# Kernel tuning notes

Hardware: AMD Instinct MI355X
Metric: run time of the kernel (lower is better)

## Reference

```python
import jax, jax.numpy as jnp
import numpy as np

R = 32          # voxel_resolution
GN_GROUPS = 8   # GroupNorm groups used throughout the module


def group_norm(x, scale, bias, groups, eps=1e-5):
    B, C = x.shape[0], x.shape[1]
    spatial = x.shape[2:]
    xg = x.reshape(B, groups, C // groups, -1)
    mu = xg.mean(axis=(2, 3), keepdims=True)
    var = xg.var(axis=(2, 3), keepdims=True)
    xn = ((xg - mu) / jnp.sqrt(var + eps)).reshape((B, C) + spatial)
    sh = (1, C) + (1,) * len(spatial)
    return xn * scale.reshape(sh) + bias.reshape(sh)


def conv3d_same(x, w, b):
    pad = w.shape[-1] // 2
    y = jax.lax.conv_general_dilated(
        x, w, (1, 1, 1), [(pad, pad)] * 3,
        dimension_numbers=('NCDHW', 'OIDHW', 'NCDHW'))
    return y + b.reshape(1, -1, 1, 1, 1)


def _voxelize(coords, features, r):
    # PVCNN Voxelization: center coords, normalize to [0,1], scale to grid,
    # scatter-MEAN point features into a dense [B,C,r,r,r] grid.
    B, C, N = features.shape
    centered = coords - coords.mean(axis=2, keepdims=True)            # [B,3,N]
    norm = jnp.linalg.norm(centered, axis=1, keepdims=True)           # [B,1,N]
    denom = norm.max(axis=2, keepdims=True) * 2.0                     # eps = 0
    nc = centered / denom + 0.5
    nc = jnp.clip(nc * r, 0.0, r - 1.0)                               # float voxel coords
    vi = jnp.round(nc).astype(jnp.int32)                              # [B,3,N]
    flat = (vi[:, 0] * r + vi[:, 1]) * r + vi[:, 2]                   # [B,N]
    seg = (flat + (jnp.arange(B, dtype=jnp.int32) * (r ** 3))[:, None]).reshape(-1)
    feats = features.transpose(0, 2, 1).reshape(B * N, C)
    sums = jax.ops.segment_sum(feats, seg, num_segments=B * r ** 3)
    cnts = jax.ops.segment_sum(jnp.ones((B * N,), feats.dtype), seg,
                               num_segments=B * r ** 3)
    mean = sums / jnp.maximum(cnts, 1.0)[:, None]
    grid = mean.reshape(B, r, r, r, C).transpose(0, 4, 1, 2, 3)       # [B,C,r,r,r]
    return nc, grid


def _trilinear_devoxelize(nc, grid, r):
    # nc [B,3,N] float in [0,r-1]; grid [B,C,r,r,r] -> gather 8 corners + weights
    B, C = grid.shape[0], grid.shape[1]
    lo = jnp.floor(nc)
    frac = nc - lo                                                    # [B,3,N]
    lo_i = lo.astype(jnp.int32)
    hi_i = jnp.minimum(lo_i + 1, r - 1)
    gf = grid.reshape(B, C, r * r * r)
    out = jnp.zeros((B, C, nc.shape[2]), grid.dtype)
    for dx in (0, 1):
        for dy in (0, 1):
            for dz in (0, 1):
                ix = hi_i[:, 0] if dx else lo_i[:, 0]
                iy = hi_i[:, 1] if dy else lo_i[:, 1]
                iz = hi_i[:, 2] if dz else lo_i[:, 2]
                w = ((frac[:, 0] if dx else 1.0 - frac[:, 0]) *
                     (frac[:, 1] if dy else 1.0 - frac[:, 1]) *
                     (frac[:, 2] if dz else 1.0 - frac[:, 2]))        # [B,N]
                idx = (ix * r + iy) * r + iz                          # [B,N]
                g = jnp.take_along_axis(gf, idx[:, None, :], axis=2)  # [B,C,N]
                out = out + g * w[:, None, :]
    return out


def setup_inputs() -> dict:
    key = jax.random.key(0)
    ks = jax.random.split(key, 6)
    B, N, Cin, Cout, K = 4, 65536, 64, 128, 3
    return {
        'coords':   jax.random.normal(ks[0], (B, 3, N), jnp.float32),
        'features': jax.random.normal(ks[1], (B, Cin, N), jnp.float32),
        'conv1_w':  jax.random.normal(ks[2], (Cout, Cin, K, K, K), jnp.float32) * 0.02,
        'conv1_b':  jnp.zeros((Cout,), jnp.float32),
        'gn1_scale': jnp.ones((Cout,), jnp.float32),
        'gn1_bias':  jnp.zeros((Cout,), jnp.float32),
        'conv2_w':  jax.random.normal(ks[3], (Cout, Cout, K, K, K), jnp.float32) * 0.02,
        'conv2_b':  jnp.zeros((Cout,), jnp.float32),
        'gn2_scale': jnp.ones((Cout,), jnp.float32),
        'gn2_bias':  jnp.zeros((Cout,), jnp.float32),
        'point_w':  jax.random.normal(ks[4], (Cout, Cin), jnp.float32) * 0.05,
        'point_b':  jnp.zeros((Cout,), jnp.float32),
        'point_gn_scale': jnp.ones((Cout,), jnp.float32),
        'point_gn_bias':  jnp.zeros((Cout,), jnp.float32),
    }


def reference(coords, features, conv1_w, conv1_b, gn1_scale, gn1_bias,
              conv2_w, conv2_b, gn2_scale, gn2_bias,
              point_w, point_b, point_gn_scale, point_gn_bias):
    nc, grid = _voxelize(coords, features, R)
    # voxel branch: Conv3d -> GN -> SiLU -> (dropout, eval: identity) -> Conv3d -> GN -> SiLU
    h = conv3d_same(grid, conv1_w, conv1_b)
    h = jax.nn.silu(group_norm(h, gn1_scale, gn1_bias, GN_GROUPS))
    h = conv3d_same(h, conv2_w, conv2_b)
    h = jax.nn.silu(group_norm(h, gn2_scale, gn2_bias, GN_GROUPS))
    # point branch: SharedMLP = 1x1 Conv1d -> GN -> SiLU
    p = jnp.einsum('oc,bcn->bon', point_w, features) + point_b[None, :, None]
    p = jax.nn.silu(group_norm(p, point_gn_scale, point_gn_bias, GN_GROUPS))
    vpts = _trilinear_devoxelize(nc, h, R)                            # [B,Cout,N]
    return p + vpts
```

## Files before the change

kernel.cpp:

```cpp
#include <hip/hip_runtime.h>

typedef __attribute__((ext_vector_type(8))) short bf16x8;
typedef __attribute__((ext_vector_type(4))) float f32x4;
typedef __attribute__((ext_vector_type(4))) int i32x4;
typedef __attribute__((ext_vector_type(2))) int i32x2;

#define B_ 4
#define N_ 65536
#define RRR_ 32768
#define PADV_ 39304
#define PPLANE_ 1156

static const size_t OFF_NC     = 0;
static const size_t OFF_VIDX   = 786432;
static const size_t OFF_WT1    = 1048576;
static const size_t OFF_WT2    = 1159168;
static const size_t OFF_C2OUT  = 1380352;
static const size_t OFF_CNT    = 9768960;
static const size_t OFF_GSUM   = 9900032;
static const size_t OFF_GPAD   = 18288640;
static const size_t OFF_ACT1   = 23319552;
static const size_t OFF_GSTATS = 33381376;
static const size_t OFF_BSTATS = 33381568;
static const size_t MEMSET_FLOATS = 33381584 - 9768960;

__device__ __forceinline__ ushort f2bf(float x) {
    union { float f; unsigned u; } c; c.f = x;
    unsigned r = c.u + 0x7fffu + ((c.u >> 16) & 1u);
    return (ushort)(r >> 16);
}
__device__ __forceinline__ float bf2f(ushort h) {
    union { unsigned u; float f; } c; c.u = ((unsigned)h) << 16;
    return c.f;
}

__device__ __forceinline__ void gl16(const void* g, void* l) {
    __builtin_amdgcn_global_load_lds(
        (const __attribute__((address_space(1))) unsigned int*)(g),
        (__attribute__((address_space(3))) unsigned int*)(l),
        16, 0, 0);
}

__global__ __launch_bounds__(256) void k_coord_sum(const float* __restrict__ coords,
                                                   float* __restrict__ bstats) {
    int b = blockIdx.y;
    int tid = threadIdx.x;
    const float* cb = coords + (size_t)b * 3 * N_;
    float s0 = 0.f, s1 = 0.f, s2 = 0.f;
    for (int n = blockIdx.x * 256 + tid; n < N_; n += 64 * 256) {
        s0 += cb[n]; s1 += cb[N_ + n]; s2 += cb[2 * N_ + n];
    }
    #pragma unroll
    for (int off = 1; off < 64; off <<= 1) {
        s0 += __shfl_xor(s0, off);
        s1 += __shfl_xor(s1, off);
        s2 += __shfl_xor(s2, off);
    }
    if ((tid & 63) == 0) {
        atomicAdd(&bstats[b * 4 + 0], s0);
        atomicAdd(&bstats[b * 4 + 1], s1);
        atomicAdd(&bstats[b * 4 + 2], s2);
    }
}

__global__ __launch_bounds__(256) void k_coord_max(const float* __restrict__ coords,
                                                   float* __restrict__ bstats) {
    int b = blockIdx.y;
    int tid = threadIdx.x;
    const float invN = 1.0f / (float)N_;
    float m0 = bstats[b * 4 + 0] * invN;
    float m1 = bstats[b * 4 + 1] * invN;
    float m2 = bstats[b * 4 + 2] * invN;
    const float* cb = coords + (size_t)b * 3 * N_;
    float mx = 0.f;
    for (int n = blockIdx.x * 256 + tid; n < N_; n += 64 * 256) {
        float x = cb[n] - m0, y = cb[N_ + n] - m1, z = cb[2 * N_ + n] - m2;
        mx = fmaxf(mx, x * x + y * y + z * z);
    }
    #pragma unroll
    for (int off = 1; off < 64; off <<= 1)
        mx = fmaxf(mx, __shfl_xor(mx, off));
    if ((tid & 63) == 0)
        atomicMax((int*)&bstats[b * 4 + 3], __float_as_int(mx));
}

__global__ __launch_bounds__(256) void k_point_prep(const float* __restrict__ coords,
                                                    const float* __restrict__ bstats,
                                                    float* __restrict__ nc,
                                                    int* __restrict__ vidx,
                                                    float* __restrict__ cnt) {
    int gid = blockIdx.x * 256 + threadIdx.x;
    int b = gid >> 16;
    int n = gid & (N_ - 1);
    const float invN = 1.0f / (float)N_;
    float m[3] = {bstats[b * 4 + 0] * invN, bstats[b * 4 + 1] * invN, bstats[b * 4 + 2] * invN};
    float den = 2.0f * sqrtf(__int_as_float(((const int*)bstats)[b * 4 + 3]));
    const float* cb = coords + (size_t)b * 3 * N_;
    int vi[3];
    #pragma unroll
    for (int d = 0; d < 3; ++d) {
        float cv = cb[(size_t)d * N_ + n];
        float t = (cv - m[d]) / den + 0.5f;
        t *= 32.0f;
        t = fminf(fmaxf(t, 0.0f), 31.0f);
        nc[((size_t)b * 3 + d) * N_ + n] = t;
        vi[d] = (int)rintf(t);
    }
    int flat = (vi[0] * 32 + vi[1]) * 32 + vi[2];
    vidx[(b << 16) + n] = flat;
    atomicAdd(&cnt[(b << 15) + flat], 1.0f);
}

__global__ __launch_bounds__(256) void k_scatter_cl(const float* __restrict__ feats,
                                                    const int* __restrict__ vidx,
                                                    float* __restrict__ gsum) {
    __shared__ float lf[64 * 129];
    __shared__ int sidx[128];
    int tid = threadIdx.x;
    int b = blockIdx.y;
    int n0 = blockIdx.x * 128;
    for (int i = tid; i < 64 * 128; i += 256) {
        int ci = i >> 7, pt = i & 127;
        lf[ci * 129 + pt] = feats[((size_t)(b * 64 + ci)) * N_ + n0 + pt];
    }
    if (tid < 128) sidx[tid] = vidx[(b << 16) + n0 + tid];
    __syncthreads();
    for (int i = tid; i < 64 * 128; i += 256) {
        int ci = i & 63, pt = i >> 6;
        atomicAdd(&gsum[((size_t)(b << 15) + sidx[pt]) * 64 + ci], lf[ci * 129 + pt]);
    }
}

__global__ __launch_bounds__(256) void k_gridmean_cl(const float* __restrict__ gsum,
                                                     const float* __restrict__ cnt,
                                                     ushort* __restrict__ gpad) {
    int idx = blockIdx.x * 256 + threadIdx.x;
    int q = idx & 15;
    int vox = (idx >> 4) & 32767;
    int b = idx >> 19;
    float c = cnt[(b << 15) + vox];
    float inv = 1.0f / fmaxf(c, 1.0f);
    float4 v = *(const float4*)(gsum + (((size_t)(b << 15) + vox) << 6) + q * 4);
    int zz = vox >> 10, yy = (vox >> 5) & 31, xx = vox & 31;
    size_t o = ((size_t)b * PADV_ + (size_t)(zz + 1) * PPLANE_ + (yy + 1) * 34 + (xx + 1)) * 64 + q * 4;
    i32x2 pk;
    ushort* u = (ushort*)&pk;
    u[0] = f2bf(v.x * inv); u[1] = f2bf(v.y * inv);
    u[2] = f2bf(v.z * inv); u[3] = f2bf(v.w * inv);
    *(i32x2*)(gpad + o) = pk;
}

template <int CI>
__global__ __launch_bounds__(256) void k_wtrans(const float* __restrict__ w,
                                                ushort* __restrict__ wt) {
    int idx = blockIdx.x * 256 + threadIdx.x;
    if (idx >= 27 * 128 * CI) return;
    int e = idx & 7;
    int jm = (idx >> 3) & 7;
    int co = (idx >> 6) & 127;
    int ks = idx >> 13;
    int q = jm ^ (co & 7);
    int tap = (CI == 64) ? ks : (ks >> 1);
    int ci = ((CI == 64) ? 0 : ((ks & 1) * 64)) + q * 8 + e;
    wt[idx] = f2bf(w[((size_t)co * CI + ci) * 27 + tap]);
}

template <int CI, bool PAD_OUT>
__global__ __launch_bounds__(256, 5) void k_conv(const ushort* __restrict__ inp,
                                                 const ushort* __restrict__ wt,
                                                 const float* __restrict__ bias,
                                                 ushort* __restrict__ outp,
                                                 float* __restrict__ gstats,
                                                 int layer) {
    constexpr int NK = 27 * CI / 64;
    __shared__ char lds[32768];

    const int yg = blockIdx.x, z0 = blockIdx.y, b = blockIdx.z;
    const int y0 = yg * 4;
    const int tid = threadIdx.x;
    const int w = tid >> 6, l = tid & 63;
    const int lk = l >> 4, lr = l & 15;
    const int wr = w >> 1, wc = w & 1;

    const char* actb = (const char*)(inp + (size_t)b * PADV_ * CI);
    const char* wtb = (const char*)wt;

    const char* agp[4];
    #pragma unroll
    for (int i = 0; i < 4; ++i) {
        int s = tid + i * 256;
        int row = s >> 3, j = s & 7;
        int jj = j ^ (row & 7);
        int py = row >> 5, px = row & 31;
        agp[i] = actb + ((size_t)(z0 * PPLANE_ + (y0 + py) * 34 + px) * CI) * 2 + jj * 16;
    }
    char* ldsAw = lds + w * 1024;
    char* ldsBw = lds + 16384 + w * 1024;

    int ard[4][2], brd[4][2];
    #pragma unroll
    for (int i = 0; i < 4; ++i) {
        int pos = wr * 64 + i * 16 + lr;
        #pragma unroll
        for (int kk = 0; kk < 2; ++kk)
            ard[i][kk] = pos * 128 + (((kk * 4 + lk) ^ (pos & 7)) << 4);
    }
    #pragma unroll
    for (int n = 0; n < 4; ++n) {
        int co = wc * 64 + n * 16 + lr;
        #pragma unroll
        for (int kk = 0; kk < 2; ++kk)
            brd[n][kk] = co * 128 + (((kk * 4 + lk) ^ (co & 7)) << 4);
    }

    f32x4 acc[4][4];
    #pragma unroll
    for (int i = 0; i < 4; ++i)
        #pragma unroll
        for (int n = 0; n < 4; ++n)
            acc[i][n] = (f32x4){0.f, 0.f, 0.f, 0.f};

    #pragma unroll 1
    for (int ks = 0; ks < NK; ++ks) {
        {
            int tap = (CI == 64) ? ks : (ks >> 1);
            int choff2 = (CI == 64) ? 0 : ((ks & 1) << 7);
            int fz = tap / 9, r9 = tap - fz * 9;
            int fy = r9 / 3, fx = r9 - fy * 3;
            int ad = (fz * PPLANE_ + fy * 34 + fx) * CI * 2 + choff2;
            #pragma unroll
            for (int i = 0; i < 4; ++i)
                gl16(agp[i] + ad, ldsAw + i * 4096);
            const char* wsrc = wtb + (size_t)ks * 16384 + tid * 16;
            #pragma unroll
            for (int i = 0; i < 4; ++i)
                gl16(wsrc + i * 4096, ldsBw + i * 4096);
        }
        __syncthreads();
        #pragma unroll
        for (int kk = 0; kk < 2; ++kk) {
            bf16x8 af[4], bfr[4];
            #pragma unroll
            for (int i = 0; i < 4; ++i) af[i] = *(const bf16x8*)(lds + ard[i][kk]);
            #pragma unroll
            for (int n = 0; n < 4; ++n) bfr[n] = *(const bf16x8*)(lds + 16384 + brd[n][kk]);
            #pragma unroll
            for (int i = 0; i < 4; ++i)
                #pragma unroll
                for (int n = 0; n < 4; ++n)
                    acc[i][n] = __builtin_amdgcn_mfma_f32_16x16x32_bf16(af[i], bfr[n], acc[i][n], 0, 0, 0);
        }
        __syncthreads();
    }

    ushort* outs = (ushort*)lds;
    float bb[4];
    #pragma unroll
    for (int n = 0; n < 4; ++n) bb[n] = bias[wc * 64 + n * 16 + lr];
    float sg[4] = {0.f, 0.f, 0.f, 0.f}, sq[4] = {0.f, 0.f, 0.f, 0.f};
    #pragma unroll
    for (int i = 0; i < 4; ++i) {
        int posb = wr * 64 + i * 16 + lk * 4;
        #pragma unroll
        for (int n = 0; n < 4; ++n) {
            int co = wc * 64 + n * 16 + lr;
            #pragma unroll
            for (int r = 0; r < 4; ++r) {
                float v = acc[i][n][r] + bb[n];
                sg[n] += v; sq[n] += v * v;
                outs[(posb + r) * 128 + co] = f2bf(v);
            }
        }
    }
    #pragma unroll
    for (int off = 1; off < 64; off <<= 1) {
        #pragma unroll
        for (int n = 0; n < 4; ++n) {
            sg[n] += __shfl_xor(sg[n], off);
            sq[n] += __shfl_xor(sq[n], off);
        }
    }
    if (l == 0) {
        int gbase = layer * 32 + b * 8 + wc * 4;
        #pragma unroll
        for (int n = 0; n < 4; ++n) {
            atomicAdd(&gstats[(gbase + n) * 2 + 0], sg[n]);
            atomicAdd(&gstats[(gbase + n) * 2 + 1], sq[n]);
        }
    }
    __syncthreads();
    for (int idx = tid; idx < 2048; idx += 256) {
        int pos = idx >> 4, c8 = idx & 15;
        int yy = y0 + (pos >> 5), xx = pos & 31;
        size_t g;
        if (PAD_OUT)
            g = ((size_t)b * PADV_ + (size_t)(z0 + 1) * PPLANE_ + (yy + 1) * 34 + (xx + 1)) * 128 + c8 * 8;
        else
            g = ((size_t)b * RRR_ + z0 * 1024 + yy * 32 + xx) * 128 + c8 * 8;
        *(i32x4*)(outp + g) = *((i32x4*)lds + idx);
    }
}

template <bool PAD>
__global__ __launch_bounds__(256) void k_gn_apply(ushort* __restrict__ x,
                                                  const float* __restrict__ gstats,
                                                  const float* __restrict__ sc,
                                                  const float* __restrict__ bi,
                                                  int layer, float invc) {
    int idx = blockIdx.x * 256 + threadIdx.x;
    int c8 = idx & 15;
    int vox = (idx >> 4) & 32767;
    int b = idx >> 19;
    size_t base;
    if (PAD) {
        int zz = vox >> 10, yy = (vox >> 5) & 31, xx = vox & 31;
        base = ((size_t)b * PADV_ + (size_t)(zz + 1) * PPLANE_ + (yy + 1) * 34 + (xx + 1)) * 128 + c8 * 8;
    } else {
        base = ((size_t)b * RRR_ + vox) * 128 + c8 * 8;
    }
    int g = c8 >> 1;
    float sum = gstats[(layer * 32 + b * 8 + g) * 2 + 0];
    float ssq = gstats[(layer * 32 + b * 8 + g) * 2 + 1];
    float mean = sum * invc;
    float var = ssq * invc - mean * mean;
    float rstd = rsqrtf(var + 1e-5f);
    i32x4 raw = *(i32x4*)(x + base);
    ushort* u = (ushort*)&raw;
    #pragma unroll
    for (int j = 0; j < 8; ++j) {
        int co = c8 * 8 + j;
        float v = bf2f(u[j]);
        v = (v - mean) * rstd * sc[co] + bi[co];
        v = v / (1.f + __expf(-v));
        u[j] = f2bf(v);
    }
    *(i32x4*)(x + base) = raw;
}

__global__ __launch_bounds__(256) void k_point_mlp(const float* __restrict__ feats,
                                                   const float* __restrict__ w,
                                                   const float* __restrict__ pb,
                                                   float* __restrict__ out,
                                                   float* __restrict__ gstats) {
    __shared__ float wl[64 * 132];
    __shared__ float sred[4][16];
    int tid = threadIdx.x;
    for (int i = tid; i < 128 * 64; i += 256) {
        int o = i >> 6, c = i & 63;
        wl[c * 132 + o] = w[i];
    }
    __syncthreads();
    int gid = blockIdx.x * 256 + tid;
    int b = gid >> 16, n = gid & (N_ - 1);
    const float* fb = feats + (size_t)b * 64 * N_ + n;
    float acc[128];
    #pragma unroll
    for (int o = 0; o < 128; ++o) acc[o] = 0.f;
    for (int c = 0; c < 64; ++c) {
        float f = fb[(size_t)c * N_];
        const float4* wr4 = (const float4*)&wl[c * 132];
        #pragma unroll
        for (int o4 = 0; o4 < 32; ++o4) {
            float4 wv = wr4[o4];
            acc[4 * o4 + 0] = fmaf(f, wv.x, acc[4 * o4 + 0]);
            acc[4 * o4 + 1] = fmaf(f, wv.y, acc[4 * o4 + 1]);
            acc[4 * o4 + 2] = fmaf(f, wv.z, acc[4 * o4 + 2]);
            acc[4 * o4 + 3] = fmaf(f, wv.w, acc[4 * o4 + 3]);
        }
    }
    float* ob = out + (size_t)b * 128 * N_ + n;
    float sg[8] = {0.f}, sq[8] = {0.f};
    #pragma unroll
    for (int o = 0; o < 128; ++o) {
        float v = acc[o] + pb[o];
        ob[(size_t)o * N_] = v;
        sg[o >> 4] += v;
        sq[o >> 4] += v * v;
    }
    #pragma unroll
    for (int off = 1; off < 64; off <<= 1) {
        #pragma unroll
        for (int g = 0; g < 8; ++g) {
            sg[g] += __shfl_xor(sg[g], off);
            sq[g] += __shfl_xor(sq[g], off);
        }
    }
    int wv = tid >> 6, l = tid & 63;
    if (l == 0) {
        #pragma unroll
        for (int g = 0; g < 8; ++g) { sred[wv][g] = sg[g]; sred[wv][8 + g] = sq[g]; }
    }
    __syncthreads();
    if (tid < 16) {
        float v = sred[0][tid] + sred[1][tid] + sred[2][tid] + sred[3][tid];
        int g = tid & 7, part = tid >> 3;
        atomicAdd(&gstats[(64 + b * 8 + g) * 2 + part], v);
    }
}

__global__ __launch_bounds__(256) void k_devox_final(const float* __restrict__ nc,
                                                     const ushort* __restrict__ ht,
                                                     const float* __restrict__ gstats,
                                                     const float* __restrict__ scale,
                                                     const float* __restrict__ bias,
                                                     float* __restrict__ out) {
    __shared__ float vp[64][129];
    __shared__ int sidx[64][8];
    __shared__ float swt[64][8];
    int tid = threadIdx.x;
    int blk = blockIdx.x;
    int b = blk >> 10;
    int n0 = (blk & 1023) * 64;
    if (tid < 64) {
        int n = n0 + tid;
        float f0 = nc[(size_t)b * 3 * N_ + n];
        float f1 = nc[((size_t)b * 3 + 1) * N_ + n];
        float f2 = nc[((size_t)b * 3 + 2) * N_ + n];
        float l0 = floorf(f0), l1 = floorf(f1), l2 = floorf(f2);
        float r0 = f0 - l0, r1 = f1 - l1, r2 = f2 - l2;
        int i0 = (int)l0, i1 = (int)l1, i2 = (int)l2;
        int h0 = min(i0 + 1, 31), h1 = min(i1 + 1, 31), h2 = min(i2 + 1, 31);
        #pragma unroll
        for (int k = 0; k < 8; ++k) {
            int dx = (k >> 2) & 1, dy = (k >> 1) & 1, dz = k & 1;
            int ix = dx ? h0 : i0, iy = dy ? h1 : i1, iz = dz ? h2 : i2;
            float w = (dx ? r0 : 1.f - r0) * (dy ? r1 : 1.f - r1) * (dz ? r2 : 1.f - r2);
            sidx[tid][k] = (ix * 32 + iy) * 32 + iz;
            swt[tid][k] = w;
        }
    }
    __syncthreads();
    const ushort* hb = ht + (size_t)b * RRR_ * 128;
    for (int t = tid; t < 64 * 16; t += 256) {
        int c8 = t & 15, pt = t >> 4;
        float a[8] = {0.f, 0.f, 0.f, 0.f, 0.f, 0.f, 0.f, 0.f};
        #pragma unroll
        for (int k = 0; k < 8; ++k) {
            i32x4 raw = *(const i32x4*)(hb + (size_t)sidx[pt][k] * 128 + c8 * 8);
            ushort* u = (ushort*)&raw;
            float wk = swt[pt][k];
            #pragma unroll
            for (int j = 0; j < 8; ++j)
                a[j] = fmaf(wk, bf2f(u[j]), a[j]);
        }
        #pragma unroll
        for (int j = 0; j < 8; ++j)
            vp[pt][c8 * 8 + j] = a[j];
    }
    __syncthreads();
    const float invc = 1.0f / (16.0f * (float)N_);
    for (int t = tid; t < 64 * 128; t += 256) {
        int nl = t & 63;
        int c = t >> 6;
        int g = c >> 4;
        float sum = gstats[(64 + b * 8 + g) * 2 + 0];
        float ssq = gstats[(64 + b * 8 + g) * 2 + 1];
        float mean = sum * invc;
        float var = ssq * invc - mean * mean;
        float rstd = rsqrtf(var + 1e-5f);
        size_t o = ((size_t)(b * 128 + c)) * N_ + n0 + nl;
        float v = (out[o] - mean) * rstd * scale[c] + bias[c];
        v = v / (1.f + __expf(-v));
        out[o] = v + vp[nl][c];
    }
}

extern "C" void kernel_launch(void* const* d_in, const int* in_sizes, int n_in,
                              void* d_out, int out_size, void* d_ws, size_t ws_size,
                              hipStream_t stream) {
    const float* coords   = (const float*)d_in[0];
    const float* features = (const float*)d_in[1];
    const float* conv1_w  = (const float*)d_in[2];
    const float* conv1_b  = (const float*)d_in[3];
    const float* gn1_s    = (const float*)d_in[4];
    const float* gn1_b    = (const float*)d_in[5];
    const float* conv2_w  = (const float*)d_in[6];
    const float* conv2_b  = (const float*)d_in[7];
    const float* gn2_s    = (const float*)d_in[8];
    const float* gn2_b    = (const float*)d_in[9];
    const float* point_w  = (const float*)d_in[10];
    const float* point_b  = (const float*)d_in[11];
    const float* pgn_s    = (const float*)d_in[12];
    const float* pgn_b    = (const float*)d_in[13];
    float* out = (float*)d_out;
    float* ws = (float*)d_ws;

    float*  nc     = ws + OFF_NC;
    int*    vidx   = (int*)(ws + OFF_VIDX);
    ushort* wt1    = (ushort*)(ws + OFF_WT1);
    ushort* wt2    = (ushort*)(ws + OFF_WT2);
    ushort* c2out  = (ushort*)(ws + OFF_C2OUT);
    float*  cnt    = ws + OFF_CNT;
    float*  gsum   = ws + OFF_GSUM;
    ushort* gpad   = (ushort*)(ws + OFF_GPAD);
    ushort* act1   = (ushort*)(ws + OFF_ACT1);
    float*  gstats = ws + OFF_GSTATS;
    float*  bstats = ws + OFF_BSTATS;

    const float invc = 1.0f / (float)(RRR_ * 16);

    hipMemsetAsync(cnt, 0, MEMSET_FLOATS * sizeof(float), stream);

    k_coord_sum<<<dim3(64, B_), 256, 0, stream>>>(coords, bstats);
    k_coord_max<<<dim3(64, B_), 256, 0, stream>>>(coords, bstats);
    k_point_prep<<<B_ * N_ / 256, 256, 0, stream>>>(coords, bstats, nc, vidx, cnt);
    k_scatter_cl<<<dim3(N_ / 128, B_), 256, 0, stream>>>(features, vidx, gsum);
    k_gridmean_cl<<<B_ * RRR_ * 16 / 256, 256, 0, stream>>>(gsum, cnt, gpad);

    k_wtrans<64><<<(27 * 128 * 64 + 255) / 256, 256, 0, stream>>>(conv1_w, wt1);
    k_wtrans<128><<<(27 * 128 * 128 + 255) / 256, 256, 0, stream>>>(conv2_w, wt2);

    k_conv<64, true><<<dim3(8, 32, B_), 256, 0, stream>>>(gpad, wt1, conv1_b, act1, gstats, 0);
    k_gn_apply<true><<<B_ * RRR_ * 16 / 256, 256, 0, stream>>>(act1, gstats, gn1_s, gn1_b, 0, invc);

    k_conv<128, false><<<dim3(8, 32, B_), 256, 0, stream>>>(act1, wt2, conv2_b, c2out, gstats, 1);
    k_gn_apply<false><<<B_ * RRR_ * 16 / 256, 256, 0, stream>>>(c2out, gstats, gn2_s, gn2_b, 1, invc);

    k_point_mlp<<<B_ * N_ / 256, 256, 0, stream>>>(features, point_w, point_b, out, gstats);
    k_devox_final<<<B_ * N_ / 64, 256, 0, stream>>>(nc, c2out, gstats, pgn_s, pgn_b, out);
}
```

Before: 1.118 ms.

## Enlarge conv tiles to 256 positions, stagger K start, store point MLP in bf16

```diff
diff --git a/kernel.cpp b/kernel.cpp
--- a/kernel.cpp
+++ b/kernel.cpp
@@ -23,6 +23,7 @@
 static const size_t OFF_GSTATS = 33381376;
 static const size_t OFF_BSTATS = 33381568;
 static const size_t MEMSET_FLOATS = 33381584 - 9768960;
+static const size_t OFF_PBF    = 9900032;
 
 __device__ __forceinline__ ushort f2bf(float x) {
     union { float f; unsigned u; } c; c.f = x;
@@ -155,63 +156,62 @@
                                                 ushort* __restrict__ wt) {
     int idx = blockIdx.x * 256 + threadIdx.x;
     if (idx >= 27 * 128 * CI) return;
-    int e = idx & 7;
-    int jm = (idx >> 3) & 7;
+    int chin = idx & 63;
     int co = (idx >> 6) & 127;
     int ks = idx >> 13;
-    int q = jm ^ (co & 7);
     int tap = (CI == 64) ? ks : (ks >> 1);
-    int ci = ((CI == 64) ? 0 : ((ks & 1) * 64)) + q * 8 + e;
+    int ci = ((CI == 64) ? 0 : ((ks & 1) * 64)) + chin;
     wt[idx] = f2bf(w[((size_t)co * CI + ci) * 27 + tap]);
 }
 
 template <int CI, bool PAD_OUT>
-__global__ __launch_bounds__(256, 5) void k_conv(const ushort* __restrict__ inp,
+__global__ __launch_bounds__(512, 4) void k_conv(const ushort* __restrict__ inp,
                                                  const ushort* __restrict__ wt,
                                                  const float* __restrict__ bias,
                                                  ushort* __restrict__ outp,
                                                  float* __restrict__ gstats,
                                                  int layer) {
     constexpr int NK = 27 * CI / 64;
-    __shared__ char lds[32768];
-
-    const int yg = blockIdx.x, z0 = blockIdx.y, b = blockIdx.z;
-    const int y0 = yg * 4;
+    __shared__ char lds[49152];
+
+    const int bid = blockIdx.x;
+    const int wid = (bid & 7) * 64 + (bid >> 3);
+    const int yg = wid & 3;
+    const int z0 = (wid >> 2) & 31;
+    const int b = wid >> 7;
+    const int y0 = yg * 8;
     const int tid = threadIdx.x;
     const int w = tid >> 6, l = tid & 63;
     const int lk = l >> 4, lr = l & 15;
     const int wr = w >> 1, wc = w & 1;
+    const int start = (wid * 7) % NK;
 
     const char* actb = (const char*)(inp + (size_t)b * PADV_ * CI);
     const char* wtb = (const char*)wt;
 
-    const char* agp[4];
+    int st_a[4];
     #pragma unroll
     for (int i = 0; i < 4; ++i) {
-        int s = tid + i * 256;
+        int s = tid + i * 512;
         int row = s >> 3, j = s & 7;
-        int jj = j ^ (row & 7);
         int py = row >> 5, px = row & 31;
-        agp[i] = actb + ((size_t)(z0 * PPLANE_ + (y0 + py) * 34 + px) * CI) * 2 + jj * 16;
-    }
-    char* ldsAw = lds + w * 1024;
-    char* ldsBw = lds + 16384 + w * 1024;
-
-    int ard[4][2], brd[4][2];
-    #pragma unroll
-    for (int i = 0; i < 4; ++i) {
-        int pos = wr * 64 + i * 16 + lr;
-        #pragma unroll
-        for (int kk = 0; kk < 2; ++kk)
-            ard[i][kk] = pos * 128 + (((kk * 4 + lk) ^ (pos & 7)) << 4);
-    }
-    #pragma unroll
-    for (int n = 0; n < 4; ++n) {
-        int co = wc * 64 + n * 16 + lr;
-        #pragma unroll
-        for (int kk = 0; kk < 2; ++kk)
-            brd[n][kk] = co * 128 + (((kk * 4 + lk) ^ (co & 7)) << 4);
-    }
+        st_a[i] = (z0 * PPLANE_ + (y0 + py) * 34 + px) * CI * 2 + ((j ^ (row & 7)) << 4);
+    }
+    int st_b[2];
+    #pragma unroll
+    for (int i = 0; i < 2; ++i) {
+        int s = tid + i * 512;
+        int co = s >> 3, j = s & 7;
+        st_b[i] = co * 128 + ((j ^ (co & 7)) << 4);
+    }
+    int swz[2];
+    #pragma unroll
+    for (int kk = 0; kk < 2; ++kk) swz[kk] = (((kk * 4 + lk) ^ (lr & 7)) << 4);
+    int apos[4], bco[4];
+    #pragma unroll
+    for (int i = 0; i < 4; ++i) apos[i] = (wr * 64 + i * 16 + lr) * 128;
+    #pragma unroll
+    for (int n = 0; n < 4; ++n) bco[n] = 32768 + (wc * 64 + n * 16 + lr) * 128;
 
     f32x4 acc[4][4];
     #pragma unroll
@@ -222,82 +222,100 @@
 
     #pragma unroll 1
     for (int ks = 0; ks < NK; ++ks) {
+        int kss = ks + start;
+        if (kss >= NK) kss -= NK;
         {
-            int tap = (CI == 64) ? ks : (ks >> 1);
-            int choff2 = (CI == 64) ? 0 : ((ks & 1) << 7);
+            int tap = (CI == 64) ? kss : (kss >> 1);
+            int choff2 = (CI == 64) ? 0 : ((kss & 1) << 7);
             int fz = tap / 9, r9 = tap - fz * 9;
             int fy = r9 / 3, fx = r9 - fy * 3;
             int ad = (fz * PPLANE_ + fy * 34 + fx) * CI * 2 + choff2;
             #pragma unroll
             for (int i = 0; i < 4; ++i)
-                gl16(agp[i] + ad, ldsAw + i * 4096);
-            const char* wsrc = wtb + (size_t)ks * 16384 + tid * 16;
-            #pragma unroll
-            for (int i = 0; i < 4; ++i)
-                gl16(wsrc + i * 4096, ldsBw + i * 4096);
+                gl16(actb + st_a[i] + ad, lds + i * 8192 + w * 1024);
+            const char* wsrc = wtb + (size_t)kss * 16384;
+            #pragma unroll
+            for (int i = 0; i < 2; ++i)
+                gl16(wsrc + st_b[i], lds + 32768 + i * 8192 + w * 1024);
         }
         __syncthreads();
         #pragma unroll
         for (int kk = 0; kk < 2; ++kk) {
-            bf16x8 af[4], bfr[4];
-            #pragma unroll
-            for (int i = 0; i < 4; ++i) af[i] = *(const bf16x8*)(lds + ard[i][kk]);
-            #pragma unroll
-            for (int n = 0; n < 4; ++n) bfr[n] = *(const bf16x8*)(lds + 16384 + brd[n][kk]);
+            bf16x8 af[4], bf[4];
+            #pragma unroll
+            for (int i = 0; i < 4; ++i) af[i] = *(const bf16x8*)(lds + apos[i] + swz[kk]);
+            #pragma unroll
+            for (int n = 0; n < 4; ++n) bf[n] = *(const bf16x8*)(lds + bco[n] + swz[kk]);
             #pragma unroll
             for (int i = 0; i < 4; ++i)
                 #pragma unroll
                 for (int n = 0; n < 4; ++n)
-                    acc[i][n] = __builtin_amdgcn_mfma_f32_16x16x32_bf16(af[i], bfr[n], acc[i][n], 0, 0, 0);
+                    acc[i][n] = __builtin_amdgcn_mfma_f32_16x16x32_bf16(af[i], bf[n], acc[i][n], 0, 0, 0);
         }
         __syncthreads();
     }
 
+    float bb[4];
+    #pragma unroll
+    for (int n = 0; n < 4; ++n) bb[n] = bias[wc * 64 + n * 16 + lr];
+    {
+        float sg[4] = {0.f, 0.f, 0.f, 0.f}, sq[4] = {0.f, 0.f, 0.f, 0.f};
+        #pragma unroll
+        for (int i = 0; i < 4; ++i)
+            #pragma unroll
+            for (int n = 0; n < 4; ++n)
+                #pragma unroll
+                for (int r = 0; r < 4; ++r) {
+                    float v = acc[i][n][r] + bb[n];
+                    sg[n] += v; sq[n] += v * v;
+                }
+        #pragma unroll
+        for (int off = 1; off < 64; off <<= 1) {
+            #pragma unroll
+            for (int n = 0; n < 4; ++n) {
+                sg[n] += __shfl_xor(sg[n], off);
+                sq[n] += __shfl_xor(sq[n], off);
+            }
+        }
+        if (l == 0) {
+            int gbase = layer * 32 + b * 8 + wc * 4;
+            #pragma unroll
+            for (int n = 0; n < 4; ++n) {
+                atomicAdd(&gstats[(gbase + n) * 2 + 0], sg[n]);
+                atomicAdd(&gstats[(gbase + n) * 2 + 1], sq[n]);
+            }
+        }
+    }
+
     ushort* outs = (ushort*)lds;
-    float bb[4];
-    #pragma unroll
-    for (int n = 0; n < 4; ++n) bb[n] = bias[wc * 64 + n * 16 + lr];
-    float sg[4] = {0.f, 0.f, 0.f, 0.f}, sq[4] = {0.f, 0.f, 0.f, 0.f};
-    #pragma unroll
-    for (int i = 0; i < 4; ++i) {
-        int posb = wr * 64 + i * 16 + lk * 4;
-        #pragma unroll
-        for (int n = 0; n < 4; ++n) {
-            int co = wc * 64 + n * 16 + lr;
-            #pragma unroll
-            for (int r = 0; r < 4; ++r) {
-                float v = acc[i][n][r] + bb[n];
-                sg[n] += v; sq[n] += v * v;
-                outs[(posb + r) * 128 + co] = f2bf(v);
+    #pragma unroll
+    for (int p = 0; p < 2; ++p) {
+        __syncthreads();
+        if ((wr >> 1) == p) {
+            #pragma unroll
+            for (int i = 0; i < 4; ++i) {
+                int posl = (wr & 1) * 64 + i * 16 + lk * 4;
+                #pragma unroll
+                for (int n = 0; n < 4; ++n) {
+                    int co = wc * 64 + n * 16 + lr;
+                    #pragma unroll
+                    for (int r = 0; r < 4; ++r)
+                        outs[(posl + r) * 128 + co] = f2bf(acc[i][n][r] + bb[n]);
+                }
             }
         }
-    }
-    #pragma unroll
-    for (int off = 1; off < 64; off <<= 1) {
-        #pragma unroll
-        for (int n = 0; n < 4; ++n) {
-            sg[n] += __shfl_xor(sg[n], off);
-            sq[n] += __shfl_xor(sq[n], off);
-        }
-    }
-    if (l == 0) {
-        int gbase = layer * 32 + b * 8 + wc * 4;
-        #pragma unroll
-        for (int n = 0; n < 4; ++n) {
-            atomicAdd(&gstats[(gbase + n) * 2 + 0], sg[n]);
-            atomicAdd(&gstats[(gbase + n) * 2 + 1], sq[n]);
-        }
-    }
-    __syncthreads();
-    for (int idx = tid; idx < 2048; idx += 256) {
-        int pos = idx >> 4, c8 = idx & 15;
-        int yy = y0 + (pos >> 5), xx = pos & 31;
-        size_t g;
-        if (PAD_OUT)
-            g = ((size_t)b * PADV_ + (size_t)(z0 + 1) * PPLANE_ + (yy + 1) * 34 + (xx + 1)) * 128 + c8 * 8;
-        else
-            g = ((size_t)b * RRR_ + z0 * 1024 + yy * 32 + xx) * 128 + c8 * 8;
-        *(i32x4*)(outp + g) = *((i32x4*)lds + idx);
+        __syncthreads();
+        for (int idx = tid; idx < 2048; idx += 512) {
+            int posl = idx >> 4, c8 = idx & 15;
+            int pos = p * 128 + posl;
+            int yy = y0 + (pos >> 5), xx = pos & 31;
+            size_t g;
+            if (PAD_OUT)
+                g = ((size_t)b * PADV_ + (size_t)(z0 + 1) * PPLANE_ + (yy + 1) * 34 + (xx + 1)) * 128 + c8 * 8;
+            else
+                g = ((size_t)b * RRR_ + z0 * 1024 + yy * 32 + xx) * 128 + c8 * 8;
+            *(i32x4*)(outp + g) = *((i32x4*)lds + idx);
+        }
     }
 }
 
@@ -340,7 +358,7 @@
 __global__ __launch_bounds__(256) void k_point_mlp(const float* __restrict__ feats,
                                                    const float* __restrict__ w,
                                                    const float* __restrict__ pb,
-                                                   float* __restrict__ out,
+                                                   ushort* __restrict__ pbf,
                                                    float* __restrict__ gstats) {
     __shared__ float wl[64 * 132];
     __shared__ float sred[4][16];
@@ -368,12 +386,12 @@
             acc[4 * o4 + 3] = fmaf(f, wv.w, acc[4 * o4 + 3]);
         }
     }
-    float* ob = out + (size_t)b * 128 * N_ + n;
+    ushort* ob = pbf + (size_t)b * 128 * N_ + n;
     float sg[8] = {0.f}, sq[8] = {0.f};
     #pragma unroll
     for (int o = 0; o < 128; ++o) {
         float v = acc[o] + pb[o];
-        ob[(size_t)o * N_] = v;
+        ob[(size_t)o * N_] = f2bf(v);
         sg[o >> 4] += v;
         sq[o >> 4] += v * v;
     }
@@ -400,6 +418,7 @@
 
 __global__ __launch_bounds__(256) void k_devox_final(const float* __restrict__ nc,
                                                      const ushort* __restrict__ ht,
+                                                     const ushort* __restrict__ pbf,
                                                      const float* __restrict__ gstats,
                                                      const float* __restrict__ scale,
                                                      const float* __restrict__ bias,
@@ -459,7 +478,7 @@
         float var = ssq * invc - mean * mean;
         float rstd = rsqrtf(var + 1e-5f);
         size_t o = ((size_t)(b * 128 + c)) * N_ + n0 + nl;
-        float v = (out[o] - mean) * rstd * scale[c] + bias[c];
+        float v = (bf2f(pbf[o]) - mean) * rstd * scale[c] + bias[c];
         v = v / (1.f + __expf(-v));
         out[o] = v + vp[nl][c];
     }
@@ -496,6 +515,7 @@
     ushort* act1   = (ushort*)(ws + OFF_ACT1);
     float*  gstats = ws + OFF_GSTATS;
     float*  bstats = ws + OFF_BSTATS;
+    ushort* pbf    = (ushort*)(ws + OFF_PBF);
 
     const float invc = 1.0f / (float)(RRR_ * 16);
 
@@ -510,12 +530,12 @@
     k_wtrans<64><<<(27 * 128 * 64 + 255) / 256, 256, 0, stream>>>(conv1_w, wt1);
     k_wtrans<128><<<(27 * 128 * 128 + 255) / 256, 256, 0, stream>>>(conv2_w, wt2);
 
-    k_conv<64, true><<<dim3(8, 32, B_), 256, 0, stream>>>(gpad, wt1, conv1_b, act1, gstats, 0);
+    k_conv<64, true><<<512, 512, 0, stream>>>(gpad, wt1, conv1_b, act1, gstats, 0);
     k_gn_apply<true><<<B_ * RRR_ * 16 / 256, 256, 0, stream>>>(act1, gstats, gn1_s, gn1_b, 0, invc);
 
-    k_conv<128, false><<<dim3(8, 32, B_), 256, 0, stream>>>(act1, wt2, conv2_b, c2out, gstats, 1);
+    k_conv<128, false><<<512, 512, 0, stream>>>(act1, wt2, conv2_b, c2out, gstats, 1);
     k_gn_apply<false><<<B_ * RRR_ * 16 / 256, 256, 0, stream>>>(c2out, gstats, gn2_s, gn2_b, 1, invc);
 
-    k_point_mlp<<<B_ * N_ / 256, 256, 0, stream>>>(features, point_w, point_b, out, gstats);
-    k_devox_final<<<B_ * N_ / 64, 256, 0, stream>>>(nc, c2out, gstats, pgn_s, pgn_b, out);
-}
+    k_point_mlp<<<B_ * N_ / 256, 256, 0, stream>>>(features, point_w, point_b, pbf, gstats);
+    k_devox_final<<<B_ * N_ / 64, 256, 0, stream>>>(nc, c2out, pbf, gstats, pgn_s, pgn_b, out);
+}
```

New measurement: 1.009 ms. -9.7%, faster.
